# Kernel tuning notes

Hardware: AMD Instinct MI355X
Metric: run time of the kernel (lower is better)

Reference implementation:

```python
import jax, jax.numpy as jnp
import numpy as np

B, D, E, H = 8192, 2048, 8, 128

def setup_inputs() -> dict:
    key = jax.random.key(0)
    ks = jax.random.split(key, 9)
    s_d = 1.0 / np.sqrt(D)
    s_h = 1.0 / np.sqrt(H)
    return {
        "x": jax.random.normal(ks[0], (B, D), dtype=jnp.float32),
        "gate_w": jax.random.normal(ks[1], (D, E), dtype=jnp.float32) * s_d,
        "gate_b": jnp.zeros((E,), dtype=jnp.float32),
        "W1": jax.random.normal(ks[2], (E, D, H), dtype=jnp.float32) * s_d,
        "b1": jnp.zeros((E, H), dtype=jnp.float32),
        "W2": jax.random.normal(ks[3], (E, H, H), dtype=jnp.float32) * s_h,
        "b2": jnp.zeros((E, H), dtype=jnp.float32),
        "W3": jax.random.normal(ks[4], (E, H, D), dtype=jnp.float32) * s_h,
        "b3": jnp.zeros((E, D), dtype=jnp.float32),
    }

def reference(x, gate_w, gate_b, W1, b1, W2, b2, W3, b3):
    # Adaptive gate: softmax over experts
    gates = jax.nn.softmax(x @ gate_w + gate_b, axis=1)          # [B, E]
    # All experts as one batched (grouped) GEMM over the expert axis.
    h1 = jax.nn.silu(jnp.einsum('bd,edh->ebh', x, W1) + b1[:, None, :])   # [E, B, H]
    h2 = jax.nn.silu(jnp.einsum('ebh,ehk->ebk', h1, W2) + b2[:, None, :]) # [E, B, H]
    y = jnp.einsum('ebh,ehd->ebd', h2, W3) + b3[:, None, :]               # [E, B, D]
    # Gate-weighted sum over experts (fused reduction, no [B,E,D] stack kept)
    out = jnp.einsum('be,ebd->bd', gates, y)                     # [B, D]
    return out
```

## Files before the change

kernel.cpp:

```cpp
#include <hip/hip_runtime.h>


typedef __attribute__((ext_vector_type(8))) short short8;
typedef __attribute__((ext_vector_type(4))) short bf16x4;
typedef __attribute__((ext_vector_type(4))) float f32x4;

#define B_SZ 8192
#define D_SZ 2048
#define E_SZ 8
#define H_SZ 128

__device__ __forceinline__ short f2bf(float f) {
  unsigned u = __builtin_bit_cast(unsigned, f);
  unsigned r = (u + 0x7fffu + ((u >> 16) & 1u)) >> 16;
  return (short)r;
}

__device__ __forceinline__ float silu_f(float v) {
  return v / (1.f + __expf(-v));
}

__device__ __forceinline__ void gload_lds16(const void* g, void* l) {
  __builtin_amdgcn_global_load_lds(
      (const __attribute__((address_space(1))) void*)g,
      (__attribute__((address_space(3))) void*)l,
      16, 0, 0);
}

template<int NHT>
__device__ __forceinline__ void core128(const short* __restrict__ A,
                                        const short* __restrict__ B,
                                        short* lds, f32x4 acc[4][4])
{
  const int tid  = threadIdx.x;
  const int lane = tid & 63;
  const int wid  = tid >> 6;
  const int wr = wid >> 1, wc = wid & 1;
  const int lm = lane & 15, lk = lane >> 4;
  const int wl = (tid & ~63) * 8;

  auto STAGE = [&](int eta) {
    const size_t go = (size_t)(eta >> 1)*8192 + (size_t)(eta & 1)*4096;
    short* l = lds + (eta & 1)*8192;
    gload_lds16(A + go + tid*8,        l + wl);
    gload_lds16(A + go + 2048 + tid*8, l + 2048 + wl);
    gload_lds16(B + go + tid*8,        l + 4096 + wl);
    gload_lds16(B + go + 2048 + tid*8, l + 6144 + wl);
  };

  STAGE(0);
  __syncthreads();
  for (int eta = 0; eta < NHT; ++eta) {
    if (eta + 1 < NHT) STAGE(eta + 1);
    const short* la = lds + (eta & 1)*8192 + lk*1024 + (wr*64 + lm)*8;
    const short* lb = lds + (eta & 1)*8192 + 4096 + lk*1024 + (wc*64 + lm)*8;
    short8 av[4], bv[4];
    #pragma unroll
    for (int f = 0; f < 4; ++f) av[f] = *(const short8*)(la + f*128);
    #pragma unroll
    for (int f = 0; f < 4; ++f) bv[f] = *(const short8*)(lb + f*128);
    #pragma unroll
    for (int i = 0; i < 4; ++i)
      #pragma unroll
      for (int j = 0; j < 4; ++j)
        acc[i][j] = __builtin_amdgcn_mfma_f32_16x16x32_bf16(av[i], bv[j], acc[i][j], 0, 0, 0);
    __syncthreads();
  }
}

__global__ __launch_bounds__(256)
void k_cvt_gate(const float* __restrict__ x,  const float* __restrict__ W1,
                const float* __restrict__ W2, const float* __restrict__ W3,
                const float* __restrict__ gw, const float* __restrict__ gb,
                short* __restrict__ xf, short* __restrict__ w1f,
                short* __restrict__ w2f, short* __restrict__ w3f,
                float* __restrict__ gates)
{
  __shared__ short lt[8192];
  const int b = blockIdx.x;
  const int tid = threadIdx.x;

  if (b < 512) {
    const int lane = tid & 63, wid = tid >> 6;
    const int row0 = b*16 + wid*4;
    float acc[4][8] = {};
    #pragma unroll
    for (int it = 0; it < 8; ++it) {
      const int k = it*256 + lane*4;
      float4 xv[4];
      #pragma unroll
      for (int r = 0; r < 4; ++r)
        xv[r] = *(const float4*)(x + (size_t)(row0 + r)*2048 + k);
      float4 gv[4][2];
      #pragma unroll
      for (int d = 0; d < 4; ++d) {
        gv[d][0] = *(const float4*)(gw + (size_t)(k + d)*8);
        gv[d][1] = *(const float4*)(gw + (size_t)(k + d)*8 + 4);
      }
      #pragma unroll
      for (int r = 0; r < 4; ++r) {
        const float xr[4] = {xv[r].x, xv[r].y, xv[r].z, xv[r].w};
        #pragma unroll
        for (int d = 0; d < 4; ++d) {
          acc[r][0] += xr[d]*gv[d][0].x; acc[r][1] += xr[d]*gv[d][0].y;
          acc[r][2] += xr[d]*gv[d][0].z; acc[r][3] += xr[d]*gv[d][0].w;
          acc[r][4] += xr[d]*gv[d][1].x; acc[r][5] += xr[d]*gv[d][1].y;
          acc[r][6] += xr[d]*gv[d][1].z; acc[r][7] += xr[d]*gv[d][1].w;
        }
      }
    }
    #pragma unroll
    for (int r = 0; r < 4; ++r)
      #pragma unroll
      for (int e = 0; e < 8; ++e)
        #pragma unroll
        for (int d = 1; d < 64; d <<= 1)
          acc[r][e] += __shfl_xor(acc[r][e], d, 64);
    if (lane < 4) {
      float lg[8], mx = -1e30f;
      #pragma unroll
      for (int e = 0; e < 8; ++e) { lg[e] = acc[lane][e] + gb[e]; mx = fmaxf(mx, lg[e]); }
      float s = 0.f;
      #pragma unroll
      for (int e = 0; e < 8; ++e) { lg[e] = __expf(lg[e] - mx); s += lg[e]; }
      const float inv = 1.f / s;
      #pragma unroll
      for (int e = 0; e < 8; ++e) gates[(size_t)(row0 + lane)*8 + e] = lg[e] * inv;
    }
  } else if (b < 2560) {
    const int t = b - 512;
    const int bt = t >> 5, kt = t & 31;
    const float* xb = x + (size_t)bt*128*2048 + kt*64;
    #pragma unroll
    for (int u = 0; u < 8; ++u) {
      const int flat = u*1024 + tid*4;
      const int row = flat >> 6, kk = flat & 63;
      const float4 v = *(const float4*)(xb + (size_t)row*2048 + kk);
      const int kg = kk >> 3;
      bf16x4 o;
      o[0] = f2bf(v.x); o[1] = f2bf(v.y); o[2] = f2bf(v.z); o[3] = f2bf(v.w);
      const int s = (kg*1024 + row*8 + (kk & 7)) ^ ((kg & 7) << 3);
      *(bf16x4*)(lt + s) = o;
    }
    __syncthreads();
    short* dst = xf + (size_t)t*8192;
    #pragma unroll
    for (int u = 0; u < 4; ++u) {
      const int li = u*2048 + tid*8;
      const int kg = li >> 10;
      const int s = li ^ ((kg & 7) << 3);
      *(short8*)(dst + li) = *(const short8*)(lt + s);
    }
  } else {
    const int gi = (b - 2560)*256 + tid + 2097152;
    if (gi < 2097152 + 262144) {
      const int g = gi - 2097152;
      const int t = g >> 10, r = g & 1023;
      const int e = t >> 5, kt = t & 31;
      const int kg = r >> 7, p = r & 127;
      const int k0 = kt*64 + kg*8;
      short8 o;
      #pragma unroll
      for (int j = 0; j < 8; ++j)
        o[j] = f2bf(W1[(size_t)e*262144 + (size_t)(k0 + j)*128 + p]);
      *(short8*)(w1f + (size_t)g*8) = o;
    } else if (gi < 2097152 + 262144 + 16384) {
      const int g = gi - (2097152 + 262144);
      const int t = g >> 10, r = g & 1023;
      const int e = t >> 1, kt = t & 1;
      const int kg = r >> 7, p = r & 127;
      const int k0 = kt*64 + kg*8;
      short8 o;
      #pragma unroll
      for (int j = 0; j < 8; ++j)
        o[j] = f2bf(W2[(size_t)e*16384 + (size_t)(k0 + j)*128 + p]);
      *(short8*)(w2f + (size_t)g*8) = o;
    } else if (gi < 2637824) {
      const int g = gi - 2375680;
      const int t = g >> 10, r = g & 1023;
      const int nt = t >> 4, kt = t & 15;
      const int kg = r >> 7, p = r & 127;
      const int k0 = kt*64 + kg*8;
      short8 o;
      #pragma unroll
      for (int j = 0; j < 8; ++j) {
        const int k = k0 + j;
        o[j] = f2bf(W3[(size_t)(k >> 7)*262144 + (size_t)(k & 127)*2048 + nt*128 + p]);
      }
      *(short8*)(w3f + (size_t)g*8) = o;
    }
  }
}

__global__ __launch_bounds__(256, 2)
void k_gemm12f(const short* __restrict__ xf, const short* __restrict__ w1f,
               const short* __restrict__ w2f,
               const float* __restrict__ b1, const float* __restrict__ b2,
               const float* __restrict__ gates, short* __restrict__ h2gf)
{
  __shared__ short lds[16384];
  const int b = blockIdx.x;
  const int xcd = b & 7, idx = b >> 3;
  const int bt = xcd*8 + (idx & 7);
  const int e  = idx >> 3;

  f32x4 acc[4][4] = {};
  core128<64>(xf  + (size_t)bt*32*8192,
              w1f + (size_t)e*32*8192,
              lds, acc);

  const int tid = threadIdx.x, lane = tid & 63, wid = tid >> 6;
  const int wr = wid >> 1, wc = wid & 1;
  const int lm = lane & 15, lk = lane >> 4, lr = lane >> 4;

  short8 bvAll[2][2][4];
  #pragma unroll
  for (int kt = 0; kt < 2; ++kt)
  #pragma unroll
  for (int ks = 0; ks < 2; ++ks)
  #pragma unroll
  for (int fn = 0; fn < 4; ++fn)
    bvAll[kt][ks][fn] = *(const short8*)(
        w2f + (size_t)e*16384 + kt*8192 + (ks*4 + lk)*1024
            + (wc*64 + fn*16 + lm)*8);

  float gv[4][4];
  #pragma unroll
  for (int fm = 0; fm < 4; ++fm)
  #pragma unroll
  for (int i = 0; i < 4; ++i)
    gv[fm][i] = gates[(size_t)(bt*128 + wr*64 + fm*16 + lr*4 + i)*8 + e];

  float b1v[4];
  #pragma unroll
  for (int fn = 0; fn < 4; ++fn) b1v[fn] = b1[e*H_SZ + wc*64 + fn*16 + lm];
  #pragma unroll
  for (int fm = 0; fm < 4; ++fm)
  #pragma unroll
  for (int i = 0; i < 4; ++i) {
    const int m = wr*64 + fm*16 + lr*4 + i;
    #pragma unroll
    for (int fn = 0; fn < 4; ++fn) {
      const int n = wc*64 + fn*16 + lm;
      const float v = silu_f(acc[fm][fn][i] + b1v[fn]);
      lds[(n >> 3)*1024 + m*8 + (n & 7)] = f2bf(v);
    }
  }
  __syncthreads();

  f32x4 acc2[4][4] = {};
  #pragma unroll
  for (int kt = 0; kt < 2; ++kt)
  #pragma unroll
  for (int ks = 0; ks < 2; ++ks) {
    short8 av[4];
    #pragma unroll
    for (int f = 0; f < 4; ++f)
      av[f] = *(const short8*)(lds + (kt*8 + ks*4 + lk)*1024 + (wr*64 + f*16 + lm)*8);
    #pragma unroll
    for (int i = 0; i < 4; ++i)
      #pragma unroll
      for (int j = 0; j < 4; ++j)
        acc2[i][j] = __builtin_amdgcn_mfma_f32_16x16x32_bf16(
            av[i], bvAll[kt][ks][j], acc2[i][j], 0, 0, 0);
  }
  __syncthreads();

  float b2v[4];
  #pragma unroll
  for (int fn = 0; fn < 4; ++fn) b2v[fn] = b2[e*H_SZ + wc*64 + fn*16 + lm];
  #pragma unroll
  for (int fm = 0; fm < 4; ++fm)
  #pragma unroll
  for (int i = 0; i < 4; ++i) {
    const int m = wr*64 + fm*16 + lr*4 + i;
    const float g = gv[fm][i];
    #pragma unroll
    for (int fn = 0; fn < 4; ++fn) {
      const int n = wc*64 + fn*16 + lm;
      const float v = silu_f(acc2[fm][fn][i] + b2v[fn]) * g;
      lds[(n >> 3)*1024 + m*8 + (n & 7)] = f2bf(v);
    }
  }
  __syncthreads();

  #pragma unroll
  for (int q = 0; q < 8; ++q) {
    const int li = q*2048 + tid*8;
    const int t2 = li >> 13, off = li & 8191;
    *(short8*)(h2gf + ((size_t)bt*16 + e*2 + t2)*8192 + off) =
        *(const short8*)(lds + li);
  }
}

__global__ __launch_bounds__(256, 4)
void k_gemm3(const short* __restrict__ h2gf, const short* __restrict__ w3f,
             const float* __restrict__ b3, const float* __restrict__ gates,
             float* __restrict__ out)
{
  __shared__ short lds[16384];
  const int b = blockIdx.x;
  const int xcd = b & 7, idx = b >> 3;
  const int bt = xcd*8 + (idx & 7);
  const int nt = idx >> 3;

  f32x4 acc[4][4] = {};
  core128<32>(h2gf + (size_t)bt*16*8192,
              w3f  + (size_t)nt*16*8192,
              lds, acc);

  const int tid = threadIdx.x, lane = tid & 63, wid = tid >> 6;
  const int wr = wid >> 1, wc = wid & 1, lm = lane & 15, lr = lane >> 4;
  float b3c[4][8];
  #pragma unroll
  for (int fn = 0; fn < 4; ++fn) {
    const int n = nt*128 + wc*64 + fn*16 + lm;
    #pragma unroll
    for (int e = 0; e < 8; ++e) b3c[fn][e] = b3[(size_t)e*D_SZ + n];
  }
  #pragma unroll
  for (int fm = 0; fm < 4; ++fm)
  #pragma unroll
  for (int i = 0; i < 4; ++i) {
    const int m = bt*128 + wr*64 + fm*16 + lr*4 + i;
    const float4 ga  = *(const float4*)(gates + (size_t)m*8);
    const float4 gbv = *(const float4*)(gates + (size_t)m*8 + 4);
    #pragma unroll
    for (int fn = 0; fn < 4; ++fn) {
      const int n = nt*128 + wc*64 + fn*16 + lm;
      const float bias = ga.x*b3c[fn][0] + ga.y*b3c[fn][1] + ga.z*b3c[fn][2] + ga.w*b3c[fn][3]
                       + gbv.x*b3c[fn][4] + gbv.y*b3c[fn][5] + gbv.z*b3c[fn][6] + gbv.w*b3c[fn][7];
      out[(size_t)m*D_SZ + n] = acc[fm][fn][i] + bias;
    }
  }
}

extern "C" void kernel_launch(void* const* d_in, const int* in_sizes, int n_in,
                              void* d_out, int out_size, void* d_ws, size_t ws_size,
                              hipStream_t stream)
{
  (void)in_sizes; (void)n_in; (void)out_size; (void)ws_size;
  const float* x  = (const float*)d_in[0];
  const float* gw = (const float*)d_in[1];
  const float* gb = (const float*)d_in[2];
  const float* W1 = (const float*)d_in[3];
  const float* b1 = (const float*)d_in[4];
  const float* W2 = (const float*)d_in[5];
  const float* b2 = (const float*)d_in[6];
  const float* W3 = (const float*)d_in[7];
  const float* b3 = (const float*)d_in[8];
  float* out = (float*)d_out;

  char* ws = (char*)d_ws;
  short* xf    = (short*)ws;  ws += (size_t)B_SZ*D_SZ*2;
  short* w1f   = (short*)ws;  ws += (size_t)E_SZ*D_SZ*H_SZ*2;
  short* w2f   = (short*)ws;  ws += (size_t)E_SZ*H_SZ*H_SZ*2;
  short* w3f   = (short*)ws;  ws += (size_t)E_SZ*H_SZ*D_SZ*2;
  float* gates = (float*)ws;  ws += (size_t)B_SZ*E_SZ*4;
  short* h2gf  = (short*)ws;  ws += (size_t)B_SZ*E_SZ*H_SZ*2;

  k_cvt_gate<<<dim3(4672), dim3(256), 0, stream>>>(x, W1, W2, W3, gw, gb,
                                                   xf, w1f, w2f, w3f, gates);
  k_gemm12f <<<dim3(512),  dim3(256), 0, stream>>>(xf, w1f, w2f, b1, b2, gates, h2gf);
  k_gemm3   <<<dim3(1024), dim3(256), 0, stream>>>(h2gf, w3f, b3, gates, out);
}
```

Measured before the change: 135.7 us.

## Halve k_gemm12f M-tile to 64 rows with inline double-buffered K loop

Replaces the shared core128 call in the fused GEMM1+GEMM2 kernel with a custom 64x128 tile loop that double-buffers A and B slices in LDS via global_load_lds. Launches twice as many blocks (1024) with smaller LDS and launch bounds raised to 4 blocks per CU, so occupancy and CU coverage go up. It also remaps blocks so the expert index is the low bits. In exchange, each W1 tile is loaded twice as often and per-wave MFMA work per LDS read shrinks.

```diff
diff --git a/kernel.cpp b/kernel.cpp
--- a/kernel.cpp
+++ b/kernel.cpp
@@ -192,26 +192,58 @@
   }
 }
 
-__global__ __launch_bounds__(256, 2)
+__global__ __launch_bounds__(256, 4)
 void k_gemm12f(const short* __restrict__ xf, const short* __restrict__ w1f,
                const short* __restrict__ w2f,
                const float* __restrict__ b1, const float* __restrict__ b2,
                const float* __restrict__ gates, short* __restrict__ h2gf)
 {
-  __shared__ short lds[16384];
+  __shared__ short lds[12288];
   const int b = blockIdx.x;
-  const int xcd = b & 7, idx = b >> 3;
-  const int bt = xcd*8 + (idx & 7);
-  const int e  = idx >> 3;
-
-  f32x4 acc[4][4] = {};
-  core128<64>(xf  + (size_t)bt*32*8192,
-              w1f + (size_t)e*32*8192,
-              lds, acc);
+  const int e   = b & 7;
+  const int bt2 = b >> 3;
 
   const int tid = threadIdx.x, lane = tid & 63, wid = tid >> 6;
-  const int wr = wid >> 1, wc = wid & 1;
+  const int wm = wid >> 1, wn = wid & 1;
   const int lm = lane & 15, lk = lane >> 4, lr = lane >> 4;
+  const int lane8 = lane * 8;
+  const int w3c = wid * 3;
+
+  const short* Ax = xf  + (size_t)(bt2 >> 1)*32*8192 + (bt2 & 1)*512;
+  const short* Bw = w1f + (size_t)e*32*8192;
+
+  auto STAGE = [&](int eta) {
+    const size_t go = (size_t)(eta >> 1)*8192 + (size_t)(eta & 1)*4096;
+    short* l = lds + (eta & 1)*6144;
+    #pragma unroll
+    for (int c = 0; c < 3; ++c) {
+      const int u = w3c + c;
+      if (u < 4)
+        gload_lds16(Ax + go + u*1024 + lane8, l + u*512);
+      else
+        gload_lds16(Bw + go + (u - 4)*512 + lane8, l + 2048 + (u - 4)*512);
+    }
+  };
+
+  f32x4 acc[2][4] = {};
+  STAGE(0);
+  __syncthreads();
+  for (int eta = 0; eta < 64; ++eta) {
+    if (eta + 1 < 64) STAGE(eta + 1);
+    const short* la = lds + (eta & 1)*6144 + lk*512 + (wm*32 + lm)*8;
+    const short* lb = lds + (eta & 1)*6144 + 2048 + lk*1024 + (wn*64 + lm)*8;
+    short8 av[2], bv[4];
+    #pragma unroll
+    for (int f = 0; f < 2; ++f) av[f] = *(const short8*)(la + f*128);
+    #pragma unroll
+    for (int f = 0; f < 4; ++f) bv[f] = *(const short8*)(lb + f*128);
+    #pragma unroll
+    for (int i = 0; i < 2; ++i)
+      #pragma unroll
+      for (int j = 0; j < 4; ++j)
+        acc[i][j] = __builtin_amdgcn_mfma_f32_16x16x32_bf16(av[i], bv[j], acc[i][j], 0, 0, 0);
+    __syncthreads();
+  }
 
   short8 bvAll[2][2][4];
   #pragma unroll
@@ -222,74 +254,76 @@
   for (int fn = 0; fn < 4; ++fn)
     bvAll[kt][ks][fn] = *(const short8*)(
         w2f + (size_t)e*16384 + kt*8192 + (ks*4 + lk)*1024
-            + (wc*64 + fn*16 + lm)*8);
-
-  float gv[4][4];
-  #pragma unroll
-  for (int fm = 0; fm < 4; ++fm)
+            + (wn*64 + fn*16 + lm)*8);
+
+  float gv[2][4];
+  #pragma unroll
+  for (int fm = 0; fm < 2; ++fm)
   #pragma unroll
   for (int i = 0; i < 4; ++i)
-    gv[fm][i] = gates[(size_t)(bt*128 + wr*64 + fm*16 + lr*4 + i)*8 + e];
+    gv[fm][i] = gates[(size_t)(bt2*64 + wm*32 + fm*16 + lr*4 + i)*8 + e];
 
   float b1v[4];
   #pragma unroll
-  for (int fn = 0; fn < 4; ++fn) b1v[fn] = b1[e*H_SZ + wc*64 + fn*16 + lm];
-  #pragma unroll
-  for (int fm = 0; fm < 4; ++fm)
+  for (int fn = 0; fn < 4; ++fn) b1v[fn] = b1[e*H_SZ + wn*64 + fn*16 + lm];
+  #pragma unroll
+  for (int fm = 0; fm < 2; ++fm)
   #pragma unroll
   for (int i = 0; i < 4; ++i) {
-    const int m = wr*64 + fm*16 + lr*4 + i;
+    const int m = wm*32 + fm*16 + lr*4 + i;
     #pragma unroll
     for (int fn = 0; fn < 4; ++fn) {
-      const int n = wc*64 + fn*16 + lm;
+      const int n = wn*64 + fn*16 + lm;
       const float v = silu_f(acc[fm][fn][i] + b1v[fn]);
-      lds[(n >> 3)*1024 + m*8 + (n & 7)] = f2bf(v);
+      lds[(n >> 3)*512 + m*8 + (n & 7)] = f2bf(v);
     }
   }
   __syncthreads();
 
-  f32x4 acc2[4][4] = {};
+  f32x4 acc2[2][4] = {};
   #pragma unroll
   for (int kt = 0; kt < 2; ++kt)
   #pragma unroll
   for (int ks = 0; ks < 2; ++ks) {
-    short8 av[4];
-    #pragma unroll
-    for (int f = 0; f < 4; ++f)
-      av[f] = *(const short8*)(lds + (kt*8 + ks*4 + lk)*1024 + (wr*64 + f*16 + lm)*8);
-    #pragma unroll
-    for (int i = 0; i < 4; ++i)
+    short8 av2[2];
+    #pragma unroll
+    for (int f = 0; f < 2; ++f)
+      av2[f] = *(const short8*)(lds + (kt*8 + ks*4 + lk)*512 + (wm*32 + f*16 + lm)*8);
+    #pragma unroll
+    for (int i = 0; i < 2; ++i)
       #pragma unroll
       for (int j = 0; j < 4; ++j)
         acc2[i][j] = __builtin_amdgcn_mfma_f32_16x16x32_bf16(
-            av[i], bvAll[kt][ks][j], acc2[i][j], 0, 0, 0);
+            av2[i], bvAll[kt][ks][j], acc2[i][j], 0, 0, 0);
   }
   __syncthreads();
 
   float b2v[4];
   #pragma unroll
-  for (int fn = 0; fn < 4; ++fn) b2v[fn] = b2[e*H_SZ + wc*64 + fn*16 + lm];
-  #pragma unroll
-  for (int fm = 0; fm < 4; ++fm)
+  for (int fn = 0; fn < 4; ++fn) b2v[fn] = b2[e*H_SZ + wn*64 + fn*16 + lm];
+  #pragma unroll
+  for (int fm = 0; fm < 2; ++fm)
   #pragma unroll
   for (int i = 0; i < 4; ++i) {
-    const int m = wr*64 + fm*16 + lr*4 + i;
+    const int m = wm*32 + fm*16 + lr*4 + i;
     const float g = gv[fm][i];
     #pragma unroll
     for (int fn = 0; fn < 4; ++fn) {
-      const int n = wc*64 + fn*16 + lm;
+      const int n = wn*64 + fn*16 + lm;
       const float v = silu_f(acc2[fm][fn][i] + b2v[fn]) * g;
-      lds[(n >> 3)*1024 + m*8 + (n & 7)] = f2bf(v);
+      lds[(n >> 3)*512 + m*8 + (n & 7)] = f2bf(v);
     }
   }
   __syncthreads();
 
-  #pragma unroll
-  for (int q = 0; q < 8; ++q) {
-    const int li = q*2048 + tid*8;
-    const int t2 = li >> 13, off = li & 8191;
-    *(short8*)(h2gf + ((size_t)bt*16 + e*2 + t2)*8192 + off) =
-        *(const short8*)(lds + li);
+  const size_t tb = ((size_t)(bt2 >> 1)*16 + e*2)*8192 + (size_t)(bt2 & 1)*512;
+  #pragma unroll
+  for (int u = 0; u < 4; ++u) {
+    const int li = u*2048 + tid*8;
+    const int kg = li >> 9;
+    const int p  = (li >> 3) & 63;
+    short* dst = h2gf + tb + (size_t)(kg >> 3)*8192 + (kg & 7)*1024 + p*8;
+    *(short8*)dst = *(const short8*)(lds + li);
   }
 }
 
@@ -361,6 +395,6 @@
 
   k_cvt_gate<<<dim3(4672), dim3(256), 0, stream>>>(x, W1, W2, W3, gw, gb,
                                                    xf, w1f, w2f, w3f, gates);
-  k_gemm12f <<<dim3(512),  dim3(256), 0, stream>>>(xf, w1f, w2f, b1, b2, gates, h2gf);
+  k_gemm12f <<<dim3(1024), dim3(256), 0, stream>>>(xf, w1f, w2f, b1, b2, gates, h2gf);
   k_gemm3   <<<dim3(1024), dim3(256), 0, stream>>>(h2gf, w3f, b3, gates, out);
 }
```

Result: slower. 145.0 us (+6.9%).
